# Kernel optimization log

Measured on AMD Instinct MI355X. Metric: run time of the kernel, lower is better.

Reference implementation:

```python
import jax, jax.numpy as jnp
import numpy as np

# Config (matches init_kwargs + Mamba2 defaults: expand=2, headdim=64, ngroups=1)
B_, C_IN, T, H, W = 4, 23, 8, 128, 128
P = 4
DM = 256
D_STATE = 16
D_CONV = 4
EXPAND = 2
D_INNER = EXPAND * DM            # 512
HEADDIM = 64
NHEADS = D_INNER // HEADDIM      # 8
CONV_DIM = D_INNER + 2 * D_STATE # 544 (ngroups=1)
D_IN_PROJ = 2 * D_INNER + 2 * D_STATE + NHEADS


def setup_inputs() -> dict:
    key = jax.random.key(0)
    ks = jax.random.split(key, 12)
    s = lambda k, shape, sc: (jax.random.normal(k, shape, jnp.float32) * sc)
    x = jax.random.normal(ks[0], (B_, C_IN, T, H, W), jnp.float32)
    patch_w = s(ks[1], (DM, C_IN, P, P), 0.05)       # Conv3d weight, depth-1 dim squeezed
    patch_b = s(ks[2], (DM,), 0.02)
    W_in = s(ks[3], (DM, D_IN_PROJ), 0.05)           # in_proj (bias=False)
    conv_w = s(ks[4], (CONV_DIM, D_CONV), 0.2)       # depthwise conv1d weight
    conv_b = s(ks[5], (CONV_DIM,), 0.02)
    dt_bias = jnp.log(jnp.expm1(jnp.exp(jax.random.uniform(ks[6], (NHEADS,), jnp.float32, jnp.log(1e-3), jnp.log(1e-1)))))
    A_log = jnp.log(jnp.arange(1, NHEADS + 1, dtype=jnp.float32))
    D_param = jnp.ones((NHEADS,), jnp.float32)
    norm_w = jnp.ones((D_INNER,), jnp.float32)
    W_out = s(ks[7], (D_INNER, DM), 0.05)            # out_proj (bias=False)
    unembed_w = s(ks[8], (DM, C_IN, P, P), 0.05)     # ConvTranspose3d weight (in,out,1,p,p)
    unembed_b = s(ks[9], (C_IN,), 0.02)
    return {"x": x, "patch_w": patch_w, "patch_b": patch_b, "W_in": W_in,
            "conv_w": conv_w, "conv_b": conv_b, "dt_bias": dt_bias, "A_log": A_log,
            "D_param": D_param, "norm_w": norm_w, "W_out": W_out,
            "unembed_w": unembed_w, "unembed_b": unembed_b}


def reference(x, patch_w, patch_b, W_in, conv_w, conv_b, dt_bias, A_log,
              D_param, norm_w, W_out, unembed_w, unembed_b):
    B, C, Tt, Hh, Ww = x.shape
    p = patch_w.shape[-1]
    Hp, Wp = Hh // p, Ww // p
    L = Tt * Hp * Wp
    # --- Conv3d patch embed (kernel (1,p,p), stride (1,p,p)) == non-overlapping patchify ---
    xr = x.reshape(B, C, Tt, Hp, p, Wp, p)
    emb = jnp.einsum('bcthiwj,dcij->bthwd', xr, patch_w) + patch_b  # [B,T,Hp,Wp,D]
    xs = emb.reshape(B, L, DM)
    # --- Mamba2 ---
    zxbcdt = xs @ W_in                                 # [B,L,2*d_inner+2*d_state+nheads]
    z = zxbcdt[:, :, :D_INNER]
    xBC = zxbcdt[:, :, D_INNER:D_INNER + CONV_DIM]
    dt = zxbcdt[:, :, D_INNER + CONV_DIM:]             # [B,L,nheads]
    # causal depthwise conv1d + silu
    xp = jnp.pad(xBC, ((0, 0), (D_CONV - 1, 0), (0, 0)))
    conv_out = conv_b + sum(xp[:, k:k + L, :] * conv_w[:, k] for k in range(D_CONV))
    xBC = jax.nn.silu(conv_out)
    xh = xBC[:, :, :D_INNER].reshape(B, L, NHEADS, HEADDIM)
    Bm = xBC[:, :, D_INNER:D_INNER + D_STATE]          # [B,L,N] (ngroups=1)
    Cm = xBC[:, :, D_INNER + D_STATE:]                 # [B,L,N]
    dt = jax.nn.softplus(dt + dt_bias)                 # [B,L,H]
    A = -jnp.exp(A_log)                                # [H]
    dA = jnp.exp(dt * A)                               # [B,L,H]
    xdt = xh * dt[..., None]                           # [B,L,H,P]
    # selective state-space scan: h_t = dA_t h_{t-1} + (dt_t x_t) B_t^T ; y_t = h_t C_t
    def step(h, inp):
        dA_t, xdt_t, B_t, C_t = inp
        h = dA_t[..., None, None] * h + jnp.einsum('bhp,bn->bhpn', xdt_t, B_t)
        y = jnp.einsum('bhpn,bn->bhp', h, C_t)
        return h, y
    inps = (dA.transpose(1, 0, 2), xdt.transpose(1, 0, 2, 3),
            Bm.transpose(1, 0, 2), Cm.transpose(1, 0, 2))
    h0 = jnp.zeros((B, NHEADS, HEADDIM, D_STATE), xs.dtype)
    _, ys = jax.lax.scan(step, h0, inps)               # [L,B,H,P]
    y = ys.transpose(1, 0, 2, 3) + D_param[None, None, :, None] * xh
    y = y.reshape(B, L, D_INNER)
    # gated RMSNorm (norm_before_gate=False): rmsnorm(y * silu(z)) * w
    yg = y * jax.nn.silu(z)
    y = yg * jax.lax.rsqrt(jnp.mean(yg * yg, axis=-1, keepdims=True) + 1e-5) * norm_w
    out_seq = y @ W_out                                # [B,L,DM]
    # --- ConvTranspose3d unembed (kernel (1,p,p), stride (1,p,p)) == un-patchify ---
    outp = out_seq.reshape(B, Tt, Hp, Wp, DM)
    un = jnp.einsum('bthwd,dcij->bcthiwj', outp, unembed_w)
    out = un.reshape(B, C, Tt, Hh, Ww) + unembed_b[None, :, None, None, None]
    return out + x
```

## Files before the change

kernel.cpp:

```cpp
#include <hip/hip_runtime.h>
#include <hip/hip_bf16.h>
#include <cstdint>
#include <cstddef>

#define B_N       4
#define C_INCH    23
#define T_N       8
#define W_IMG     128
#define L_SEQ     8192
#define BLROWS    32768
#define DM_       256
#define D_INNER_  512
#define CONV_DIM_ 544
#define D_PROJ    1064
#define KPATCH    368
#define QCH       64
#define NCH       128

typedef unsigned short ushort_t;
typedef unsigned int uint_t;
typedef __attribute__((ext_vector_type(8))) short short8;
typedef __attribute__((ext_vector_type(4))) float f32x4;

__device__ __forceinline__ float b2f(ushort_t u) {
    union { float f; uint_t u; } v; v.u = ((uint_t)u) << 16; return v.f;
}
__device__ __forceinline__ ushort_t f2b(float f) {
    union { float f; uint_t u; } v; v.f = f;
    uint_t r = v.u + 0x7fffu + ((v.u >> 16) & 1u);
    return (ushort_t)(r >> 16);
}

__device__ __forceinline__ void gload_lds16(const ushort_t* g, ushort_t* l) {
    __builtin_amdgcn_global_load_lds(
        (const __attribute__((address_space(1))) unsigned int*)g,
        (__attribute__((address_space(3))) unsigned int*)l, 16, 0, 0);
}

__global__ void k_transcast(const float* __restrict__ src, ushort_t* __restrict__ dst,
                            int K, int N, const float* __restrict__ rscale) {
    int n = blockIdx.x;
    for (int k = threadIdx.x; k < K; k += 256) {
        float v = 0.f;
        if (n < N) {
            v = src[(size_t)k * N + n];
            if (rscale) v *= rscale[k];
        }
        dst[(size_t)n * K + k] = f2b(v);
    }
}

__global__ void k_castpad(const float* __restrict__ src, ushort_t* __restrict__ dst) {
    int d = blockIdx.x; int k = threadIdx.x;
    dst[d * 384 + k] = (k < KPATCH) ? f2b(src[d * KPATCH + k]) : (ushort_t)0;
}

__global__ void __launch_bounds__(256) k_im2col(const float* __restrict__ x,
                                                ushort_t* __restrict__ Aim) {
    int hp = blockIdx.x, t = blockIdx.y, b = blockIdx.z;
    int tid = threadIdx.x;
    int half = tid >> 7, q = tid & 127;
    int wp = q >> 2, j = q & 3;
    size_t rowbase = (size_t)b * L_SEQ + t * 1024 + hp * 32;
    #pragma unroll
    for (int it = 0; it < 2; ++it) {
        int idx = it * 256 + tid;
        int wpz = idx >> 4, kz = KPATCH + (idx & 15);
        Aim[(rowbase + wpz) * 384 + kz] = 0;
    }
    for (int s2 = 0; s2 < 46; ++s2) {
        int seg = s2 * 2 + half;
        int c = seg >> 2, i = seg & 3;
        float v = x[(((size_t)(b * C_INCH + c) * T_N + t) << 14) + (size_t)(hp * 4 + i) * W_IMG + q];
        Aim[(rowbase + wp) * 384 + c * 16 + i * 4 + j] = f2b(v);
    }
}

template <int K, int N, bool CBF>
__global__ void __launch_bounds__(256) k_mgemm(const ushort_t* __restrict__ A, const int lda,
                                               const ushort_t* __restrict__ Wt,
                                               void* __restrict__ Cv, const int ldc, const int coff,
                                               const float* __restrict__ bias,
                                               const float* __restrict__ rowscale) {
    __shared__ ushort_t Al[128 * 64];
    __shared__ ushort_t Bl[128 * 64];
    const int tid = threadIdx.x;
    const int w = tid >> 6, lane = tid & 63;
    const int wr = w >> 1, wc = w & 1;
    const int rowbase = blockIdx.y * 128;
    const int colbase = blockIdx.x * 128;
    const int g = lane >> 4, r = lane & 15;

    f32x4 acc[4][4];
    #pragma unroll
    for (int i = 0; i < 4; ++i)
        #pragma unroll
        for (int j = 0; j < 4; ++j) acc[i][j] = (f32x4){0.f, 0.f, 0.f, 0.f};

    for (int k0 = 0; k0 < K; k0 += 64) {
        __syncthreads();
        #pragma unroll
        for (int it = 0; it < 4; ++it) {
            int s = it * 256 + (w << 6) + lane;
            int row = s >> 3;
            int c16 = (s & 7) ^ (row & 7);
            gload_lds16(A + (size_t)(rowbase + row) * lda + k0 + c16 * 8,
                        &Al[(size_t)(it * 256 + (w << 6)) * 8]);
        }
        #pragma unroll
        for (int it = 0; it < 4; ++it) {
            int s = it * 256 + (w << 6) + lane;
            int row = s >> 3;
            int c16 = (s & 7) ^ (row & 7);
            gload_lds16(Wt + (size_t)(colbase + row) * K + k0 + c16 * 8,
                        &Bl[(size_t)(it * 256 + (w << 6)) * 8]);
        }
        __syncthreads();

        short8 af[2][4], bf[2][4];
        #pragma unroll
        for (int ks = 0; ks < 2; ++ks)
            #pragma unroll
            for (int mi = 0; mi < 4; ++mi) {
                int row = (wr << 6) + (mi << 4) + r;
                int c16 = ((ks << 2) | g) ^ (row & 7);
                af[ks][mi] = *(const short8*)&Al[(size_t)((row << 3) + c16) * 8];
            }
        #pragma unroll
        for (int ks = 0; ks < 2; ++ks)
            #pragma unroll
            for (int ni = 0; ni < 4; ++ni) {
                int row = (wc << 6) + (ni << 4) + r;
                int c16 = ((ks << 2) | g) ^ (row & 7);
                bf[ks][ni] = *(const short8*)&Bl[(size_t)((row << 3) + c16) * 8];
            }
        #pragma unroll
        for (int ks = 0; ks < 2; ++ks)
            #pragma unroll
            for (int mi = 0; mi < 4; ++mi)
                #pragma unroll
                for (int ni = 0; ni < 4; ++ni)
                    acc[mi][ni] = __builtin_amdgcn_mfma_f32_16x16x32_bf16(
                        af[ks][mi], bf[ks][ni], acc[mi][ni], 0, 0, 0);
    }

    #pragma unroll
    for (int mi = 0; mi < 4; ++mi) {
        int rw = rowbase + (wr << 6) + (mi << 4) + (g << 2);
        float s0 = 1.f, s1 = 1.f, s2 = 1.f, s3 = 1.f;
        if (rowscale) { s0 = rowscale[rw]; s1 = rowscale[rw+1]; s2 = rowscale[rw+2]; s3 = rowscale[rw+3]; }
        #pragma unroll
        for (int ni = 0; ni < 4; ++ni) {
            int col = colbase + (wc << 6) + (ni << 4) + r;
            if (col < N) {
                float bv = bias ? bias[col] : 0.f;
                f32x4 v = acc[mi][ni];
                float vr[4] = {v[0]*s0 + bv, v[1]*s1 + bv, v[2]*s2 + bv, v[3]*s3 + bv};
                #pragma unroll
                for (int j = 0; j < 4; ++j) {
                    size_t cidx = (size_t)(rw + j) * ldc + coff + col;
                    if (CBF) ((ushort_t*)Cv)[cidx] = f2b(vr[j]);
                    else     ((float*)Cv)[cidx]   = vr[j];
                }
            }
        }
    }
}

__global__ void __launch_bounds__(256) k_conv(const ushort_t* __restrict__ xbcdt,
                                              const float* __restrict__ cw,
                                              const float* __restrict__ cb,
                                              const float* __restrict__ dtb,
                                              const float* __restrict__ alog,
                                              ushort_t* __restrict__ xbc,
                                              float* __restrict__ bc32,
                                              float* __restrict__ dtv,
                                              float* __restrict__ dAv) {
    int tid = threadIdx.x;
    int rb = blockIdx.x * 8;
    int srb = rb & (L_SEQ - 1);
    #pragma unroll
    for (int it = 0; it < 3; ++it) {
        int ch = it * 256 + tid;
        if (ch >= 552) break;
        if (ch < CONV_DIM_) {
            float w0 = cw[ch * 4 + 0], w1 = cw[ch * 4 + 1];
            float w2 = cw[ch * 4 + 2], w3 = cw[ch * 4 + 3];
            float bias = cb[ch];
            float win[11];
            #pragma unroll
            for (int j = 0; j < 11; ++j) {
                int sj = srb + j - 3;
                win[j] = (sj >= 0) ? b2f(xbcdt[(size_t)(rb + j - 3) * 640 + ch]) : 0.f;
            }
            #pragma unroll
            for (int r = 0; r < 8; ++r) {
                float acc = bias + win[r] * w0 + win[r + 1] * w1 + win[r + 2] * w2 + win[r + 3] * w3;
                float s = acc / (1.f + __expf(-acc));
                size_t row = rb + r;
                if (ch < 512) xbc[row * 512 + ch] = f2b(s);
                else          bc32[row * 32 + (ch - 512)] = s;
            }
        } else {
            int h = ch - CONV_DIM_;
            float A = -__expf(alog[h]);
            float db = dtb[h];
            #pragma unroll
            for (int r = 0; r < 8; ++r) {
                size_t row = rb + r;
                float v = b2f(xbcdt[row * 640 + ch]) + db;
                float sp = (v > 20.f) ? v : log1pf(__expf(v));
                dtv[row * 8 + h] = sp;
                dAv[row * 8 + h] = __expf(sp * A);
            }
        }
    }
}

__global__ void __launch_bounds__(256) k_scan1(const ushort_t* __restrict__ xbc,
                                               const float* __restrict__ bc32,
                                               const float* __restrict__ dtv,
                                               const float* __restrict__ dAv,
                                               float* __restrict__ sbuf,
                                               float* __restrict__ cdf) {
    int c = blockIdx.x, b = blockIdx.z;
    int tid = threadIdx.x;
    int h = blockIdx.y * 4 + (tid >> 6);
    int p = tid & 63;
    float st[16];
    #pragma unroll
    for (int n = 0; n < 16; ++n) st[n] = 0.f;
    float cd = 1.f;
    size_t row0 = (size_t)b * L_SEQ + (size_t)c * QCH;
    for (int s = 0; s < QCH; ++s) {
        size_t row = row0 + s;
        float da  = dAv[row * 8 + h];
        float dtt = dtv[row * 8 + h];
        float xh  = b2f(xbc[row * 512 + h * 64 + p]);
        const float4* B4 = (const float4*)(bc32 + row * 32);
        float xdt = xh * dtt;
        #pragma unroll
        for (int q = 0; q < 4; ++q) {
            float4 Bv = B4[q];
            st[q*4+0] = da * st[q*4+0] + xdt * Bv.x;
            st[q*4+1] = da * st[q*4+1] + xdt * Bv.y;
            st[q*4+2] = da * st[q*4+2] + xdt * Bv.z;
            st[q*4+3] = da * st[q*4+3] + xdt * Bv.w;
        }
        cd *= da;
    }
    size_t base = (size_t)((b * 8 + h) * NCH + c) * 1024 + p * 16;
    #pragma unroll
    for (int q = 0; q < 4; ++q)
        *(float4*)&sbuf[base + q * 4] = make_float4(st[q*4], st[q*4+1], st[q*4+2], st[q*4+3]);
    if (p == 0) cdf[(b * 8 + h) * NCH + c] = cd;
}

__global__ void __launch_bounds__(256) k_chain(const float* __restrict__ sbuf,
                                               const float* __restrict__ cdf,
                                               float* __restrict__ hin) {
    int h = blockIdx.x, b = blockIdx.y;
    int tid = threadIdx.x;
    float4 H = make_float4(0.f, 0.f, 0.f, 0.f);
    size_t base = (size_t)((b * 8 + h) * NCH) * 1024;
    for (int c = 0; c < NCH; ++c) {
        *(float4*)&hin[base + (size_t)c * 1024 + tid * 4] = H;
        float cdfv = cdf[(b * 8 + h) * NCH + c];
        float4 S = *(const float4*)&sbuf[base + (size_t)c * 1024 + tid * 4];
        H.x = cdfv * H.x + S.x;
        H.y = cdfv * H.y + S.y;
        H.z = cdfv * H.z + S.z;
        H.w = cdfv * H.w + S.w;
    }
}

__global__ void __launch_bounds__(512) k_scan2(const ushort_t* __restrict__ xbc,
                                               const ushort_t* __restrict__ z_bf,
                                               const float* __restrict__ bc32,
                                               const float* __restrict__ dtv,
                                               const float* __restrict__ dAv,
                                               const float* __restrict__ Dp,
                                               const float* __restrict__ hin,
                                               ushort_t* __restrict__ yg_out) {
    int c = blockIdx.x, b = blockIdx.y;
    int tid = threadIdx.x;
    int h = tid >> 6, p = tid & 63;
    int off = h * 64 + p;
    float st[16];
    const float4* H = (const float4*)&hin[(size_t)((b * 8 + h) * NCH + c) * 1024 + p * 16];
    #pragma unroll
    for (int q = 0; q < 4; ++q) {
        float4 Hv = H[q];
        st[q*4+0] = Hv.x; st[q*4+1] = Hv.y; st[q*4+2] = Hv.z; st[q*4+3] = Hv.w;
    }
    float Dh = Dp[h];
    size_t row = (size_t)b * L_SEQ + (size_t)c * QCH;

    float da  = dAv[row * 8 + h];
    float dtt = dtv[row * 8 + h];
    float xh  = b2f(xbc[row * 512 + off]);
    float zz  = b2f(z_bf[row * 512 + off]);
    float4 Bc[4], Cc[4];
    {
        const float4* B4 = (const float4*)(bc32 + row * 32);
        #pragma unroll
        for (int q = 0; q < 4; ++q) { Bc[q] = B4[q]; Cc[q] = B4[q + 4]; }
    }

    for (int s = 0; s < QCH; ++s) {
        size_t rn = row + 1;
        float da_n  = dAv[rn * 8 + h];
        float dt_n  = dtv[rn * 8 + h];
        float xh_n  = b2f(xbc[rn * 512 + off]);
        float zz_n  = b2f(z_bf[rn * 512 + off]);
        float4 Bn[4], Cn[4];
        const float4* B4n = (const float4*)(bc32 + rn * 32);
        #pragma unroll
        for (int q = 0; q < 4; ++q) { Bn[q] = B4n[q]; Cn[q] = B4n[q + 4]; }

        float xdt = xh * dtt;
        float d0 = 0.f, d1 = 0.f, d2 = 0.f, d3 = 0.f;
        #pragma unroll
        for (int q = 0; q < 4; ++q) {
            st[q*4+0] = da * st[q*4+0] + xdt * Bc[q].x;
            st[q*4+1] = da * st[q*4+1] + xdt * Bc[q].y;
            st[q*4+2] = da * st[q*4+2] + xdt * Bc[q].z;
            st[q*4+3] = da * st[q*4+3] + xdt * Bc[q].w;
            d0 += st[q*4+0] * Cc[q].x;
            d1 += st[q*4+1] * Cc[q].y;
            d2 += st[q*4+2] * Cc[q].z;
            d3 += st[q*4+3] * Cc[q].w;
        }
        float y = (d0 + d1) + (d2 + d3) + Dh * xh;
        float yg = y * (zz / (1.f + __expf(-zz)));
        yg_out[row * 512 + off] = f2b(yg);

        row = rn; da = da_n; dtt = dt_n; xh = xh_n; zz = zz_n;
        #pragma unroll
        for (int q = 0; q < 4; ++q) { Bc[q] = Bn[q]; Cc[q] = Cn[q]; }
    }
}

__global__ void __launch_bounds__(256) k_rsum(const ushort_t* __restrict__ yg,
                                              float* __restrict__ scale) {
    int wid = threadIdx.x >> 6, lane = threadIdx.x & 63;
    int row = blockIdx.x * 4 + wid;
    short8 v = *(const short8*)&yg[(size_t)row * 512 + lane * 8];
    float s = 0.f;
    #pragma unroll
    for (int j = 0; j < 8; ++j) {
        float f = b2f((ushort_t)v[j]);
        s += f * f;
    }
    #pragma unroll
    for (int off = 32; off >= 1; off >>= 1) s += __shfl_xor(s, off);
    if (lane == 0) scale[row] = rsqrtf(s * (1.f / 512.f) + 1e-5f);
}

__global__ void __launch_bounds__(256) k_scatter(const ushort_t* __restrict__ tmp,
                                                 const float* __restrict__ ub,
                                                 const float* __restrict__ xin,
                                                 float* __restrict__ out) {
    int tid = threadIdx.x;
    int w = tid & 127;
    int h = (blockIdx.x << 1) | (tid >> 7);
    int c = blockIdx.y >> 3, t = blockIdx.y & 7;
    int b = blockIdx.z;
    size_t row = (size_t)b * L_SEQ + t * 1024 + (h >> 2) * 32 + (w >> 2);
    int kk = c * 16 + (h & 3) * 4 + (w & 3);
    size_t oidx = (((size_t)(b * C_INCH + c) * T_N + t) << 14) + (size_t)h * W_IMG + w;
    out[oidx] = b2f(tmp[row * KPATCH + kk]) + ub[c] + xin[oidx];
}

extern "C" void kernel_launch(void* const* d_in, const int* in_sizes, int n_in,
                              void* d_out, int out_size, void* d_ws, size_t ws_size,
                              hipStream_t stream) {
    const float* x       = (const float*)d_in[0];
    const float* patch_w = (const float*)d_in[1];
    const float* patch_b = (const float*)d_in[2];
    const float* W_in    = (const float*)d_in[3];
    const float* conv_w  = (const float*)d_in[4];
    const float* conv_b  = (const float*)d_in[5];
    const float* dt_bias = (const float*)d_in[6];
    const float* A_log   = (const float*)d_in[7];
    const float* D_param = (const float*)d_in[8];
    const float* norm_w  = (const float*)d_in[9];
    const float* W_out   = (const float*)d_in[10];
    const float* unemb_w = (const float*)d_in[11];
    const float* unemb_b = (const float*)d_in[12];
    float* out = (float*)d_out;

    char* p = (char*)d_ws;
    ushort_t* scratch = (ushort_t*)p; p += (size_t)BLROWS * 384 * 2;
    float* dtv  = (float*)p;   p += (size_t)BLROWS * 8 * 4;
    float* dAv  = (float*)p;   p += (size_t)BLROWS * 8 * 4;
    float* scale= (float*)p;   p += (size_t)BLROWS * 4;
    float* cdf  = (float*)p;   p += (size_t)32 * NCH * 4;
    float* sbuf = (float*)p;   p += (size_t)32 * NCH * 1024 * 4;
    float* hin  = (float*)p;   p += (size_t)32 * NCH * 1024 * 4;
    float* bc32 = (float*)p;   p += (size_t)BLROWS * 32 * 4;
    ushort_t* Wt_p   = (ushort_t*)p; p += (size_t)256 * 384 * 2;
    ushort_t* Wt_in  = (ushort_t*)p; p += (size_t)1152 * 256 * 2;
    ushort_t* Wt_out = (ushort_t*)p; p += (size_t)256 * 512 * 2;
    ushort_t* Wt_un  = (ushort_t*)p; p += (size_t)384 * 256 * 2;
    ushort_t* xs     = (ushort_t*)p; p += (size_t)BLROWS * DM_ * 2;
    ushort_t* xbc    = (ushort_t*)p; p += (size_t)BLROWS * 512 * 2;
    ushort_t* z_bf   = (ushort_t*)p; p += (size_t)BLROWS * 512 * 2;
    ushort_t* xbcdt  = (ushort_t*)p; p += (size_t)BLROWS * 640 * 2;
    size_t need = (size_t)(p - (char*)d_ws);
    if (ws_size < need) return;

    ushort_t* Aim = scratch;
    ushort_t* tmp = scratch;
    ushort_t* yg  = xbcdt;

    k_castpad<<<256, 384, 0, stream>>>(patch_w, Wt_p);
    k_transcast<<<1152, 256, 0, stream>>>(W_in, Wt_in, 256, 1064, nullptr);
    k_transcast<<<256, 256, 0, stream>>>(W_out, Wt_out, 512, 256, norm_w);
    k_transcast<<<384, 256, 0, stream>>>(unemb_w, Wt_un, 256, 368, nullptr);

    k_im2col<<<dim3(32, 8, 4), 256, 0, stream>>>(x, Aim);
    k_mgemm<384, 256, true><<<dim3(2, 256), 256, 0, stream>>>(Aim, 384, Wt_p, xs, 256, 0, patch_b, nullptr);

    k_mgemm<256, 512, true><<<dim3(4, 256), 256, 0, stream>>>(xs, 256, Wt_in, z_bf, 512, 0, nullptr, nullptr);
    k_mgemm<256, 552, true><<<dim3(5, 256), 256, 0, stream>>>(xs, 256, Wt_in + (size_t)512 * 256, xbcdt, 640, 0, nullptr, nullptr);

    k_conv<<<BLROWS / 8, 256, 0, stream>>>(xbcdt, conv_w, conv_b, dt_bias, A_log, xbc, bc32, dtv, dAv);

    k_scan1<<<dim3(NCH, 2, 4), 256, 0, stream>>>(xbc, bc32, dtv, dAv, sbuf, cdf);
    k_chain<<<dim3(8, 4), 256, 0, stream>>>(sbuf, cdf, hin);
    k_scan2<<<dim3(NCH, 4), 512, 0, stream>>>(xbc, z_bf, bc32, dtv, dAv, D_param, hin, yg);
    k_rsum<<<BLROWS / 4, 256, 0, stream>>>(yg, scale);

    k_mgemm<512, 256, true><<<dim3(2, 256), 256, 0, stream>>>(yg, 512, Wt_out, xs, DM_, 0, nullptr, scale);

    k_mgemm<256, 368, true><<<dim3(3, 256), 256, 0, stream>>>(xs, 256, Wt_un, tmp, KPATCH, 0, nullptr, nullptr);

    k_scatter<<<dim3(64, 184, 4), 256, 0, stream>>>(tmp, unemb_b, x, out);
}
```

Before: 287.0 us.

## Pack per-row B/C/dA/dt into one record and stage chunks in LDS for scans

The conv kernel now writes B, C, dA and dt into a single 48-float record per row instead of three separate arrays. Both scan kernels cooperatively copy the 64-row chunk of records into shared memory up front, then read them from LDS inside the serial recurrence. scan1 also prefetches the next xh value. This replaces scattered global loads on the serial critical path with LDS reads, at the cost of extra shared memory per block and a barrier.

```diff
diff --git a/kernel.cpp b/kernel.cpp
--- a/kernel.cpp
+++ b/kernel.cpp
@@ -16,6 +16,7 @@
 #define KPATCH    368
 #define QCH       64
 #define NCH       128
+#define RECW      48
 
 typedef unsigned short ushort_t;
 typedef unsigned int uint_t;
@@ -173,7 +174,7 @@
                                               const float* __restrict__ dtb,
                                               const float* __restrict__ alog,
                                               ushort_t* __restrict__ xbc,
-                                              float* __restrict__ bc32,
+                                              float* __restrict__ brec,
                                               float* __restrict__ dtv,
                                               float* __restrict__ dAv) {
     int tid = threadIdx.x;
@@ -199,7 +200,7 @@
                 float s = acc / (1.f + __expf(-acc));
                 size_t row = rb + r;
                 if (ch < 512) xbc[row * 512 + ch] = f2b(s);
-                else          bc32[row * 32 + (ch - 512)] = s;
+                else          brec[row * RECW + (ch - 512)] = s;
             }
         } else {
             int h = ch - CONV_DIM_;
@@ -210,35 +211,44 @@
                 size_t row = rb + r;
                 float v = b2f(xbcdt[row * 640 + ch]) + db;
                 float sp = (v > 20.f) ? v : log1pf(__expf(v));
-                dtv[row * 8 + h] = sp;
-                dAv[row * 8 + h] = __expf(sp * A);
+                brec[row * RECW + 32 + h] = __expf(sp * A);
+                brec[row * RECW + 40 + h] = sp;
             }
         }
     }
 }
 
 __global__ void __launch_bounds__(256) k_scan1(const ushort_t* __restrict__ xbc,
-                                               const float* __restrict__ bc32,
-                                               const float* __restrict__ dtv,
-                                               const float* __restrict__ dAv,
+                                               const float* __restrict__ brec,
                                                float* __restrict__ sbuf,
                                                float* __restrict__ cdf) {
+    __shared__ float rec[QCH * RECW];
     int c = blockIdx.x, b = blockIdx.z;
     int tid = threadIdx.x;
     int h = blockIdx.y * 4 + (tid >> 6);
     int p = tid & 63;
+    size_t row0 = (size_t)b * L_SEQ + (size_t)c * QCH;
+
+    {
+        const float4* src = (const float4*)(brec + row0 * RECW);
+        float4* dst = (float4*)rec;
+        #pragma unroll
+        for (int i = 0; i < 3; ++i) dst[i * 256 + tid] = src[i * 256 + tid];
+    }
+    __syncthreads();
+
     float st[16];
     #pragma unroll
     for (int n = 0; n < 16; ++n) st[n] = 0.f;
     float cd = 1.f;
-    size_t row0 = (size_t)b * L_SEQ + (size_t)c * QCH;
+    float xh = b2f(xbc[row0 * 512 + h * 64 + p]);
     for (int s = 0; s < QCH; ++s) {
-        size_t row = row0 + s;
-        float da  = dAv[row * 8 + h];
-        float dtt = dtv[row * 8 + h];
-        float xh  = b2f(xbc[row * 512 + h * 64 + p]);
-        const float4* B4 = (const float4*)(bc32 + row * 32);
+        float xh_n = b2f(xbc[(row0 + s + 1) * 512 + h * 64 + p]);
+        const float* r = rec + s * RECW;
+        float da  = r[32 + h];
+        float dtt = r[40 + h];
         float xdt = xh * dtt;
+        const float4* B4 = (const float4*)r;
         #pragma unroll
         for (int q = 0; q < 4; ++q) {
             float4 Bv = B4[q];
@@ -248,6 +258,7 @@
             st[q*4+3] = da * st[q*4+3] + xdt * Bv.w;
         }
         cd *= da;
+        xh = xh_n;
     }
     size_t base = (size_t)((b * 8 + h) * NCH + c) * 1024 + p * 16;
     #pragma unroll
@@ -276,16 +287,24 @@
 
 __global__ void __launch_bounds__(512) k_scan2(const ushort_t* __restrict__ xbc,
                                                const ushort_t* __restrict__ z_bf,
-                                               const float* __restrict__ bc32,
-                                               const float* __restrict__ dtv,
-                                               const float* __restrict__ dAv,
+                                               const float* __restrict__ brec,
                                                const float* __restrict__ Dp,
                                                const float* __restrict__ hin,
                                                ushort_t* __restrict__ yg_out) {
+    __shared__ float rec[QCH * RECW];
     int c = blockIdx.x, b = blockIdx.y;
     int tid = threadIdx.x;
     int h = tid >> 6, p = tid & 63;
     int off = h * 64 + p;
+    size_t row0 = (size_t)b * L_SEQ + (size_t)c * QCH;
+
+    {
+        const float4* src = (const float4*)(brec + row0 * RECW);
+        float4* dst = (float4*)rec;
+        dst[tid] = src[tid];
+        if (tid < 256) dst[512 + tid] = src[512 + tid];
+    }
+
     float st[16];
     const float4* H = (const float4*)&hin[(size_t)((b * 8 + h) * NCH + c) * 1024 + p * 16];
     #pragma unroll
@@ -294,50 +313,41 @@
         st[q*4+0] = Hv.x; st[q*4+1] = Hv.y; st[q*4+2] = Hv.z; st[q*4+3] = Hv.w;
     }
     float Dh = Dp[h];
-    size_t row = (size_t)b * L_SEQ + (size_t)c * QCH;
-
-    float da  = dAv[row * 8 + h];
-    float dtt = dtv[row * 8 + h];
-    float xh  = b2f(xbc[row * 512 + off]);
-    float zz  = b2f(z_bf[row * 512 + off]);
-    float4 Bc[4], Cc[4];
-    {
-        const float4* B4 = (const float4*)(bc32 + row * 32);
-        #pragma unroll
-        for (int q = 0; q < 4; ++q) { Bc[q] = B4[q]; Cc[q] = B4[q + 4]; }
-    }
-
+    float xh = b2f(xbc[row0 * 512 + off]);
+    float zz = b2f(z_bf[row0 * 512 + off]);
+    __syncthreads();
+
+    size_t row = row0;
     for (int s = 0; s < QCH; ++s) {
         size_t rn = row + 1;
-        float da_n  = dAv[rn * 8 + h];
-        float dt_n  = dtv[rn * 8 + h];
-        float xh_n  = b2f(xbc[rn * 512 + off]);
-        float zz_n  = b2f(z_bf[rn * 512 + off]);
-        float4 Bn[4], Cn[4];
-        const float4* B4n = (const float4*)(bc32 + rn * 32);
-        #pragma unroll
-        for (int q = 0; q < 4; ++q) { Bn[q] = B4n[q]; Cn[q] = B4n[q + 4]; }
-
+        float xh_n = b2f(xbc[rn * 512 + off]);
+        float zz_n = b2f(z_bf[rn * 512 + off]);
+
+        const float* r = rec + s * RECW;
+        float da  = r[32 + h];
+        float dtt = r[40 + h];
         float xdt = xh * dtt;
+        const float4* B4 = (const float4*)r;
+        const float4* C4 = (const float4*)(r + 16);
         float d0 = 0.f, d1 = 0.f, d2 = 0.f, d3 = 0.f;
         #pragma unroll
         for (int q = 0; q < 4; ++q) {
-            st[q*4+0] = da * st[q*4+0] + xdt * Bc[q].x;
-            st[q*4+1] = da * st[q*4+1] + xdt * Bc[q].y;
-            st[q*4+2] = da * st[q*4+2] + xdt * Bc[q].z;
-            st[q*4+3] = da * st[q*4+3] + xdt * Bc[q].w;
-            d0 += st[q*4+0] * Cc[q].x;
-            d1 += st[q*4+1] * Cc[q].y;
-            d2 += st[q*4+2] * Cc[q].z;
-            d3 += st[q*4+3] * Cc[q].w;
+            float4 Bv = B4[q];
+            float4 Cv = C4[q];
+            st[q*4+0] = da * st[q*4+0] + xdt * Bv.x;
+            st[q*4+1] = da * st[q*4+1] + xdt * Bv.y;
+            st[q*4+2] = da * st[q*4+2] + xdt * Bv.z;
+            st[q*4+3] = da * st[q*4+3] + xdt * Bv.w;
+            d0 += st[q*4+0] * Cv.x;
+            d1 += st[q*4+1] * Cv.y;
+            d2 += st[q*4+2] * Cv.z;
+            d3 += st[q*4+3] * Cv.w;
         }
         float y = (d0 + d1) + (d2 + d3) + Dh * xh;
         float yg = y * (zz / (1.f + __expf(-zz)));
         yg_out[row * 512 + off] = f2b(yg);
 
-        row = rn; da = da_n; dtt = dt_n; xh = xh_n; zz = zz_n;
-        #pragma unroll
-        for (int q = 0; q < 4; ++q) { Bc[q] = Bn[q]; Cc[q] = Cn[q]; }
+        row = rn; xh = xh_n; zz = zz_n;
     }
 }
 
@@ -392,13 +402,11 @@
 
     char* p = (char*)d_ws;
     ushort_t* scratch = (ushort_t*)p; p += (size_t)BLROWS * 384 * 2;
-    float* dtv  = (float*)p;   p += (size_t)BLROWS * 8 * 4;
-    float* dAv  = (float*)p;   p += (size_t)BLROWS * 8 * 4;
     float* scale= (float*)p;   p += (size_t)BLROWS * 4;
     float* cdf  = (float*)p;   p += (size_t)32 * NCH * 4;
     float* sbuf = (float*)p;   p += (size_t)32 * NCH * 1024 * 4;
     float* hin  = (float*)p;   p += (size_t)32 * NCH * 1024 * 4;
-    float* bc32 = (float*)p;   p += (size_t)BLROWS * 32 * 4;
+    float* brec = (float*)p;   p += (size_t)BLROWS * RECW * 4;
     ushort_t* Wt_p   = (ushort_t*)p; p += (size_t)256 * 384 * 2;
     ushort_t* Wt_in  = (ushort_t*)p; p += (size_t)1152 * 256 * 2;
     ushort_t* Wt_out = (ushort_t*)p; p += (size_t)256 * 512 * 2;
@@ -425,11 +433,11 @@
     k_mgemm<256, 512, true><<<dim3(4, 256), 256, 0, stream>>>(xs, 256, Wt_in, z_bf, 512, 0, nullptr, nullptr);
     k_mgemm<256, 552, true><<<dim3(5, 256), 256, 0, stream>>>(xs, 256, Wt_in + (size_t)512 * 256, xbcdt, 640, 0, nullptr, nullptr);
 
-    k_conv<<<BLROWS / 8, 256, 0, stream>>>(xbcdt, conv_w, conv_b, dt_bias, A_log, xbc, bc32, dtv, dAv);
-
-    k_scan1<<<dim3(NCH, 2, 4), 256, 0, stream>>>(xbc, bc32, dtv, dAv, sbuf, cdf);
+    k_conv<<<BLROWS / 8, 256, 0, stream>>>(xbcdt, conv_w, conv_b, dt_bias, A_log, xbc, brec, nullptr, nullptr);
+
+    k_scan1<<<dim3(NCH, 2, 4), 256, 0, stream>>>(xbc, brec, sbuf, cdf);
     k_chain<<<dim3(8, 4), 256, 0, stream>>>(sbuf, cdf, hin);
-    k_scan2<<<dim3(NCH, 4), 512, 0, stream>>>(xbc, z_bf, bc32, dtv, dAv, D_param, hin, yg);
+    k_scan2<<<dim3(NCH, 4), 512, 0, stream>>>(xbc, z_bf, brec, D_param, hin, yg);
     k_rsum<<<BLROWS / 4, 256, 0, stream>>>(yg, scale);
 
     k_mgemm<512, 256, true><<<dim3(2, 256), 256, 0, stream>>>(yg, 512, Wt_out, xs, DM_, 0, nullptr, scale);
```

New measurement: 290.4 us. No clear change (+1.2%).
